# Kernel optimization log

Measured on AMD Instinct MI355X. Metric: run time of the kernel, lower is better.

The kernel has to match this reference:

```python
import jax, jax.numpy as jnp
import numpy as np

B, S, D = 4, 2048, 768

def setup_inputs() -> dict:
    key = jax.random.key(0)
    ks = jax.random.split(key, 7)
    scale = 1.0 / np.sqrt(D)
    x = jax.random.normal(ks[0], (B, S, D), dtype=jnp.float32)
    Wq = jax.random.uniform(ks[1], (D, D), jnp.float32, -scale, scale)
    bq = jax.random.uniform(ks[2], (D,), jnp.float32, -scale, scale)
    Wk = jax.random.uniform(ks[3], (D, D), jnp.float32, -scale, scale)
    bk = jax.random.uniform(ks[4], (D,), jnp.float32, -scale, scale)
    Wv = jax.random.uniform(ks[5], (D, D), jnp.float32, -scale, scale)
    bv = jax.random.uniform(ks[6], (D,), jnp.float32, -scale, scale)
    return {"x": x, "Wq": Wq, "bq": bq, "Wk": Wk, "bk": bk, "Wv": Wv, "bv": bv}

def reference(x, Wq, bq, Wk, bk, Wv, bv):
    d = x.shape[-1]
    q = jnp.einsum('bsd,de->bse', x, Wq) + bq
    k = jnp.einsum('bsd,de->bse', x, Wk) + bk
    v = jnp.einsum('bsd,de->bse', x, Wv) + bv
    scores = jnp.einsum('bqd,bkd->bqk', q, k) / jnp.sqrt(jnp.asarray(d, x.dtype))
    attn = jax.nn.softmax(scores, axis=-1)  # [B,S,S]
    return jnp.einsum('bqk,bkd->bqd', attn, v)
```

## Files before the change

### kernel.cpp

```cpp
#include <hip/hip_runtime.h>
#include <hip/hip_bf16.h>


typedef __attribute__((ext_vector_type(8))) short short8;
typedef __attribute__((ext_vector_type(4))) short short4v;
typedef __attribute__((ext_vector_type(4))) float float4v;

static constexpr int B_ = 4, S_ = 2048, D_ = 768;
static constexpr int MS = B_ * S_;

__device__ inline short f2bf(float f) {
  __hip_bfloat16 h = __float2bfloat16(f);
  union { __hip_bfloat16 h; short s; } u; u.h = h; return u.s;
}
__device__ inline float bf2f(short s) {
  union { unsigned int u; float f; } c;
  c.u = ((unsigned int)(unsigned short)s) << 16; return c.f;
}

typedef const __attribute__((address_space(1))) unsigned int g_u32;
typedef __attribute__((address_space(3))) unsigned int l_u32;

__device__ __forceinline__ void glds16(const short* g, short* l) {
  __builtin_amdgcn_global_load_lds((g_u32*)g, (l_u32*)l, 16, 0, 0);
}

__global__ __launch_bounds__(256)
void cast_f32_bf16(const float* __restrict__ x, short* __restrict__ y, int n) {
  int i = (blockIdx.x * 256 + threadIdx.x) * 4;
  if (i + 3 < n) {
    float4v v = *(const float4v*)(x + i);
    short4v o;
    o.x = f2bf(v.x); o.y = f2bf(v.y); o.z = f2bf(v.z); o.w = f2bf(v.w);
    *(short4v*)(y + i) = o;
  }
}

__global__ void transpose_cast_w(const float* __restrict__ W0, const float* __restrict__ W1,
                                 const float* __restrict__ W2,
                                 short* __restrict__ T0, short* __restrict__ T1,
                                 short* __restrict__ T2) {
  const float* W = blockIdx.z == 0 ? W0 : (blockIdx.z == 1 ? W1 : W2);
  short* T = blockIdx.z == 0 ? T0 : (blockIdx.z == 1 ? T1 : T2);
  __shared__ float tile[32][33];
  int bx = blockIdx.x * 32, by = blockIdx.y * 32;
  int tx = threadIdx.x, ty = threadIdx.y;
  for (int r = ty; r < 32; r += 8)
    tile[r][tx] = W[(by + r) * D_ + bx + tx];
  __syncthreads();
  for (int r = ty; r < 32; r += 8)
    T[(bx + r) * D_ + by + tx] = f2bf(tile[tx][r]);
}

template<int EPI, int TM, int TN>
__global__ __launch_bounds__(256)
void gemm_bt(const short* __restrict__ A, const short* __restrict__ Bt,
             void* __restrict__ C0v, short* __restrict__ C1, short* __restrict__ C2,
             const float* __restrict__ bias0, const float* __restrict__ bias1,
             const float* __restrict__ bias2, float* __restrict__ rowsum,
             int K, int lda, int ldb, int ldc,
             long sA, long sB, long sC, float scale) {
  constexpr int BMv = TM * 32, BNv = TN * 32;
  const int b = blockIdx.z;
  A += (long)b * sA;
  Bt += (long)b * sB;
  float* Cf = (float*)C0v + (long)b * sC;
  short* Cs = (short*)C0v + (long)b * sC;
  float* rowsum_b = rowsum + (long)b * S_;

  __shared__ short As[BMv * 64];
  __shared__ short Bs[BNv * 64];

  const int t = threadIdx.x;
  const int wave = t >> 6, lane = t & 63;
  const int lane16 = lane & 15, q = lane >> 4;
  const int m0 = blockIdx.y * BMv, n0 = blockIdx.x * BNv;
  const int wm = (wave >> 1) * (TM * 16), wn = (wave & 1) * (TN * 16);
  const int rsub = lane >> 3;
  const int g = (lane & 7) ^ rsub;

  auto stage = [&](int kk) {
#pragma unroll
    for (int i = wave; i < BMv / 8; i += 4)
      glds16(A + (long)(m0 + i * 8 + rsub) * lda + kk + g * 8, &As[i * 512]);
#pragma unroll
    for (int i = wave; i < BNv / 8; i += 4)
      glds16(Bt + (long)(n0 + i * 8 + rsub) * ldb + kk + g * 8, &Bs[i * 512]);
  };

  stage(0);

  float4v acc[TM][TN];
#pragma unroll
  for (int i = 0; i < TM; i++)
#pragma unroll
    for (int j = 0; j < TN; j++) acc[i][j] = {0.f, 0.f, 0.f, 0.f};

  for (int k0 = 0; k0 < K; k0 += 64) {
    __syncthreads();

    short8 af[2][TM], bfr[2][TN];
#pragma unroll
    for (int s = 0; s < 2; s++) {
#pragma unroll
      for (int i = 0; i < TM; i++) {
        int R = wm + i * 16 + lane16;
        af[s][i] = *(const short8*)&As[R * 64 + (((s * 4 + q) ^ (R & 7)) * 8)];
      }
#pragma unroll
      for (int j = 0; j < TN; j++) {
        int R = wn + j * 16 + lane16;
        bfr[s][j] = *(const short8*)&Bs[R * 64 + (((s * 4 + q) ^ (R & 7)) * 8)];
      }
    }
    __syncthreads();

    if (k0 + 64 < K) stage(k0 + 64);

#pragma unroll
    for (int s = 0; s < 2; s++)
#pragma unroll
      for (int i = 0; i < TM; i++)
#pragma unroll
        for (int j = 0; j < TN; j++)
          acc[i][j] = __builtin_amdgcn_mfma_f32_16x16x32_bf16(af[s][i], bfr[s][j], acc[i][j], 0, 0, 0);
  }

#pragma unroll
  for (int i = 0; i < TM; i++) {
    int mrow = m0 + wm + i * 16 + q * 4;
    if (EPI == 0) {
#pragma unroll
      for (int j = 0; j < TN; j++) {
        int ncol = n0 + wn + j * 16 + lane16;
        if (ncol < 1536) {
          short* dst = ncol < 768 ? Cs : C1;
          const float* bs = ncol < 768 ? bias0 : bias1;
          int c = ncol < 768 ? ncol : ncol - 768;
#pragma unroll
          for (int rr = 0; rr < 4; rr++)
            dst[(long)(mrow + rr) * 768 + c] = f2bf(acc[i][j][rr] + bs[c]);
        } else {
          int e = ncol - 1536;
          float bv = bias2[e];
          short4v o;
#pragma unroll
          for (int rr = 0; rr < 4; rr++) o[rr] = f2bf(acc[i][j][rr] + bv);
          *(short4v*)&C2[(long)e * MS + mrow] = o;
        }
      }
    } else if (EPI == 2) {
#pragma unroll
      for (int rr = 0; rr < 4; rr++) {
        float rsumv = 0.f;
#pragma unroll
        for (int j = 0; j < TN; j++) {
          int ncol = n0 + wn + j * 16 + lane16;
          short sv = f2bf(__expf(acc[i][j][rr] * scale));
          Cs[(long)(mrow + rr) * ldc + ncol] = sv;
          rsumv += bf2f(sv);
        }
        for (int off = 1; off < 16; off <<= 1) rsumv += __shfl_xor(rsumv, off);
        if (lane16 == 0) atomicAdd(&rowsum_b[mrow + rr], rsumv);
      }
    } else {
#pragma unroll
      for (int rr = 0; rr < 4; rr++) {
        float inv = 1.0f / rowsum_b[mrow + rr];
#pragma unroll
        for (int j = 0; j < TN; j++) {
          int ncol = n0 + wn + j * 16 + lane16;
          Cf[(long)(mrow + rr) * ldc + ncol] = acc[i][j][rr] * inv;
        }
      }
    }
  }
}

extern "C" void kernel_launch(void* const* d_in, const int* in_sizes, int n_in,
                              void* d_out, int out_size, void* d_ws, size_t ws_size,
                              hipStream_t stream) {
  const float* x  = (const float*)d_in[0];
  const float* Wq = (const float*)d_in[1];
  const float* bq = (const float*)d_in[2];
  const float* Wk = (const float*)d_in[3];
  const float* bk = (const float*)d_in[4];
  const float* Wv = (const float*)d_in[5];
  const float* bv = (const float*)d_in[6];
  float* out = (float*)d_out;

  short* Xb  = (short*)d_ws;
  short* WqT = Xb + (long)MS * D_;
  short* WkT = WqT + (long)D_ * D_;
  short* WvT = WkT + (long)D_ * D_;
  short* Qb  = WvT + (long)D_ * D_;
  short* Kb  = Qb + (long)MS * D_;
  short* Vt  = Kb + (long)MS * D_;
  short* Es  = Vt + (long)MS * D_;
  float* rowsum = (float*)(Es + (long)B_ * S_ * S_);

  hipMemsetAsync(rowsum, 0, MS * sizeof(float), stream);
  cast_f32_bf16<<<(MS * D_) / 1024, 256, 0, stream>>>(x, Xb, MS * D_);
  transpose_cast_w<<<dim3(24, 24, 3), dim3(32, 8), 0, stream>>>(Wq, Wk, Wv, WqT, WkT, WvT);

  gemm_bt<0, 2, 4><<<dim3(2304 / 128, MS / 64, 1), 256, 0, stream>>>(
      Xb, WqT, Qb, Kb, Vt, bq, bk, bv, nullptr,
      D_, D_, D_, D_, 0, 0, 0, 1.0f);
  gemm_bt<2, 4, 4><<<dim3(S_ / 128, S_ / 128, B_), 256, 0, stream>>>(
      Qb, Kb, Es, nullptr, nullptr, nullptr, nullptr, nullptr, rowsum,
      D_, D_, D_, S_,
      (long)S_ * D_, (long)S_ * D_, (long)S_ * S_, 1.0f / sqrtf((float)D_));
  gemm_bt<3, 2, 4><<<dim3(D_ / 128, S_ / 64, B_), 256, 0, stream>>>(
      Es, Vt, out, nullptr, nullptr, nullptr, nullptr, nullptr, rowsum,
      S_, S_, MS, D_,
      (long)S_ * S_, (long)S_, (long)S_ * D_, 1.0f);
}
```

Baseline: 213.3 us.

## Compute softmax row sums via MFMA with ones vector in PV GEMM

Removes the atomic rowsum accumulation from the QK^T exp epilogue and the memset. The PV GEMM now computes each row's denominator itself by running an extra MFMA of the exp tile against a vector of bf16 ones, which drops the shuffles, atomics and global rowsum traffic. The projection and PV GEMMs also move to larger 128-row tiles. The cost is extra MFMA work in the PV kernel (TM per TN×TM step), recomputed redundantly in each column block, and fewer blocks per launch.

```diff
diff --git a/kernel.cpp b/kernel.cpp
--- a/kernel.cpp
+++ b/kernel.cpp
@@ -57,7 +57,7 @@
 void gemm_bt(const short* __restrict__ A, const short* __restrict__ Bt,
              void* __restrict__ C0v, short* __restrict__ C1, short* __restrict__ C2,
              const float* __restrict__ bias0, const float* __restrict__ bias1,
-             const float* __restrict__ bias2, float* __restrict__ rowsum,
+             const float* __restrict__ bias2,
              int K, int lda, int ldb, int ldc,
              long sA, long sB, long sC, float scale) {
   constexpr int BMv = TM * 32, BNv = TN * 32;
@@ -66,7 +66,6 @@
   Bt += (long)b * sB;
   float* Cf = (float*)C0v + (long)b * sC;
   short* Cs = (short*)C0v + (long)b * sC;
-  float* rowsum_b = rowsum + (long)b * S_;
 
   __shared__ short As[BMv * 64];
   __shared__ short Bs[BNv * 64];
@@ -96,6 +95,13 @@
 #pragma unroll
     for (int j = 0; j < TN; j++) acc[i][j] = {0.f, 0.f, 0.f, 0.f};
 
+  float4v acc_rs[TM];
+#pragma unroll
+  for (int i = 0; i < TM; i++) acc_rs[i] = {0.f, 0.f, 0.f, 0.f};
+  short8 ones;
+#pragma unroll
+  for (int e = 0; e < 8; e++) ones[e] = (short)0x3F80;
+
   for (int k0 = 0; k0 < K; k0 += 64) {
     __syncthreads();
 
@@ -118,12 +124,16 @@
     if (k0 + 64 < K) stage(k0 + 64);
 
 #pragma unroll
-    for (int s = 0; s < 2; s++)
-#pragma unroll
-      for (int i = 0; i < TM; i++)
+    for (int s = 0; s < 2; s++) {
+#pragma unroll
+      for (int i = 0; i < TM; i++) {
 #pragma unroll
         for (int j = 0; j < TN; j++)
           acc[i][j] = __builtin_amdgcn_mfma_f32_16x16x32_bf16(af[s][i], bfr[s][j], acc[i][j], 0, 0, 0);
+        if (EPI == 3)
+          acc_rs[i] = __builtin_amdgcn_mfma_f32_16x16x32_bf16(af[s][i], ones, acc_rs[i], 0, 0, 0);
+      }
+    }
   }
 
 #pragma unroll
@@ -151,22 +161,16 @@
       }
     } else if (EPI == 2) {
 #pragma unroll
+      for (int j = 0; j < TN; j++) {
+        int ncol = n0 + wn + j * 16 + lane16;
+#pragma unroll
+        for (int rr = 0; rr < 4; rr++)
+          Cs[(long)(mrow + rr) * ldc + ncol] = f2bf(__expf(acc[i][j][rr] * scale));
+      }
+    } else {
+#pragma unroll
       for (int rr = 0; rr < 4; rr++) {
-        float rsumv = 0.f;
-#pragma unroll
-        for (int j = 0; j < TN; j++) {
-          int ncol = n0 + wn + j * 16 + lane16;
-          short sv = f2bf(__expf(acc[i][j][rr] * scale));
-          Cs[(long)(mrow + rr) * ldc + ncol] = sv;
-          rsumv += bf2f(sv);
-        }
-        for (int off = 1; off < 16; off <<= 1) rsumv += __shfl_xor(rsumv, off);
-        if (lane16 == 0) atomicAdd(&rowsum_b[mrow + rr], rsumv);
-      }
-    } else {
-#pragma unroll
-      for (int rr = 0; rr < 4; rr++) {
-        float inv = 1.0f / rowsum_b[mrow + rr];
+        float inv = 1.0f / acc_rs[i][rr];
 #pragma unroll
         for (int j = 0; j < TN; j++) {
           int ncol = n0 + wn + j * 16 + lane16;
@@ -197,21 +201,19 @@
   short* Kb  = Qb + (long)MS * D_;
   short* Vt  = Kb + (long)MS * D_;
   short* Es  = Vt + (long)MS * D_;
-  float* rowsum = (float*)(Es + (long)B_ * S_ * S_);
-
-  hipMemsetAsync(rowsum, 0, MS * sizeof(float), stream);
+
   cast_f32_bf16<<<(MS * D_) / 1024, 256, 0, stream>>>(x, Xb, MS * D_);
   transpose_cast_w<<<dim3(24, 24, 3), dim3(32, 8), 0, stream>>>(Wq, Wk, Wv, WqT, WkT, WvT);
 
-  gemm_bt<0, 2, 4><<<dim3(2304 / 128, MS / 64, 1), 256, 0, stream>>>(
-      Xb, WqT, Qb, Kb, Vt, bq, bk, bv, nullptr,
+  gemm_bt<0, 4, 4><<<dim3(2304 / 128, MS / 128, 1), 256, 0, stream>>>(
+      Xb, WqT, Qb, Kb, Vt, bq, bk, bv,
       D_, D_, D_, D_, 0, 0, 0, 1.0f);
   gemm_bt<2, 4, 4><<<dim3(S_ / 128, S_ / 128, B_), 256, 0, stream>>>(
-      Qb, Kb, Es, nullptr, nullptr, nullptr, nullptr, nullptr, rowsum,
+      Qb, Kb, Es, nullptr, nullptr, nullptr, nullptr, nullptr,
       D_, D_, D_, S_,
       (long)S_ * D_, (long)S_ * D_, (long)S_ * S_, 1.0f / sqrtf((float)D_));
-  gemm_bt<3, 2, 4><<<dim3(D_ / 128, S_ / 64, B_), 256, 0, stream>>>(
-      Es, Vt, out, nullptr, nullptr, nullptr, nullptr, nullptr, rowsum,
+  gemm_bt<3, 4, 4><<<dim3(D_ / 128, S_ / 128, B_), 256, 0, stream>>>(
+      Es, Vt, out, nullptr, nullptr, nullptr, nullptr, nullptr,
       S_, S_, MS, D_,
       (long)S_ * S_, (long)S_, (long)S_ * D_, 1.0f);
 }
```

Result: faster. 201.9 us (-5.3%).
